# Performance work log

Hardware: AMD Instinct MI355X
Metric: run time of the kernel (lower is better)

The kernel has to match this reference:

```python
import jax, jax.numpy as jnp
import numpy as np

P = 2; NH = 8; NW = 4; NB = 6; D = 512; HID = 2048; NREG = 1; T = 1000; NACT = 3
HH = 32; WW = 32; C = 3; B = 1; DUR = 6


def _kron_bool(a, b):
    # kron(A,B)[i*p+k, j*q+l] = A[i,j] & B[k,l]
    m, n = a.shape; p, q = b.shape
    return (a[:, None, :, None] & b[None, :, None, :]).reshape(m * p, n * q)


def _masks(dur_zr, seq_zr, dur_xa, seq_xa):
    m_left = _kron_bool(jnp.eye(dur_zr, dtype=bool), jnp.ones((seq_zr, seq_zr), dtype=bool))
    tmp = jnp.ones((dur_zr, dur_zr), dtype=bool)
    band = jnp.tril(tmp, -1) ^ jnp.tril(tmp, -1 - NW)  # sliding window over previous frames
    m_right = _kron_bool(band[:, :-1], jnp.ones((seq_zr, seq_xa), dtype=bool))
    m_self = _kron_bool(jnp.tril(jnp.ones((dur_xa, dur_xa), dtype=bool)), jnp.ones((seq_xa, seq_xa), dtype=bool))
    return ~jnp.concatenate([m_left, m_right], axis=1), ~m_self


def _ln(x):
    mu = jnp.mean(x, -1, keepdims=True)
    xc = x - mu
    var = jnp.mean(xc * xc, -1, keepdims=True)
    return xc * jax.lax.rsqrt(var + 1e-5)


def _patch(x, Wp, bp):
    b, dur, c, h, w = x.shape
    x = x.reshape(b, dur, c, h // P, P, w // P, P)
    x = x.transpose(0, 1, 3, 5, 2, 4, 6).reshape(b, dur, (h // P) * (w // P), c * P * P)
    return x @ Wp + bp


def _unpatch(x, Wu, bu):
    b, dur, s, d = x.shape
    y = x @ Wu + bu  # [b,dur,s,C*P*P]
    y = y.reshape(b, dur, HH // P, WW // P, C, P, P)
    return y.transpose(0, 1, 4, 2, 5, 3, 6).reshape(b, dur, C, HH, WW)


def _mod(x, cond, Wm, bm):
    # AdaLN: per-frame scale/shift broadcast over tokens of that frame
    scale, shift = jnp.split(jax.nn.silu(cond) @ Wm + bm, 2, axis=-1)
    b, L, d = x.shape; dur = cond.shape[1]; s = L // dur
    y = _ln(x).reshape(b, dur, s, d)
    return (y * (1.0 + scale[:, :, None]) + shift[:, :, None]).reshape(b, L, d)


def _gate(x, cond, Wg, bg):
    g = cond @ Wg + bg
    b, L, d = x.shape; dur = cond.shape[1]; s = L // dur
    return (x.reshape(b, dur, s, d) * g[:, :, None]).reshape(b, L, d)


def _attn(q, kv, mask, Wq, bq, Wk, bk, Wv, bv, Wo, bo):
    b, lq, d = q.shape; lk = kv.shape[1]; dh = d // NH
    qh = (q @ Wq + bq).reshape(b, lq, NH, dh)
    kh = (kv @ Wk + bk).reshape(b, lk, NH, dh)
    vh = (kv @ Wv + bv).reshape(b, lk, NH, dh)
    s = jnp.einsum('bqhd,bkhd->bhqk', qh, kh) * (1.0 / np.sqrt(dh))
    s = jnp.where(mask[None, None], -1e9, s)  # mask True = disallowed
    o = jnp.einsum('bhqk,bkhd->bqhd', jax.nn.softmax(s, axis=-1), vh)
    return o.reshape(b, lq, d) @ Wo + bo


def _geglu(x, Wg, bg, Wo, bo):
    a, g = jnp.split(x @ Wg + bg, 2, axis=-1)
    return (a * jax.nn.gelu(g, approximate=False)) @ Wo + bo


def _forward(z, frames, actions, ts, W_patch, b_patch, W_unpatch, b_unpatch, registers, pe_grid, action_emb, time_emb, W_mod1, b_mod1, W_mod2, b_mod2, W_q, b_q, W_k, b_k, W_v, b_v, W_o, b_o, W_g1, b_g1, W_g2, b_g2, W_geglu, b_geglu, W_ffout, b_ffout):
    zt = _patch(z, W_patch, b_patch) + pe_grid[None, None]
    xt = _patch(frames, W_patch, b_patch) + pe_grid[None, None]
    a = action_emb[actions]  # [B, dur, D]
    b, dur_zr, s, d = zt.shape
    zr = jnp.concatenate([zt, jnp.broadcast_to(registers[None, None], (b, dur_zr, NREG, d))], axis=2)
    xa = jnp.concatenate([xt, a[:, :-1, None, :]], axis=2)
    seq_zr = zr.shape[2]; dur_xa = xa.shape[1]; seq_xa = xa.shape[2]
    mask_cross, mask_self = _masks(dur_zr, seq_zr, dur_xa, seq_xa)
    zr = zr.reshape(b, dur_zr * seq_zr, d)
    xa = xa.reshape(b, dur_xa * seq_xa, d)
    cond = time_emb[ts]  # [B, dur_zr, D]
    clean = jnp.broadcast_to(time_emb[0][None, None], (b, dur_xa, d))
    for i in range(NB):
        zrn = _mod(zr, cond, W_mod1[i], b_mod1[i])
        xan = _mod(xa, clean, W_mod1[i], b_mod1[i])
        xkv = jnp.concatenate([zrn, xan], axis=1)
        cross = _attn(zrn, xkv, mask_cross, W_q[i], b_q[i], W_k[i], b_k[i], W_v[i], b_v[i], W_o[i], b_o[i])
        selfa = _attn(xan, xan, mask_self, W_q[i], b_q[i], W_k[i], b_k[i], W_v[i], b_v[i], W_o[i], b_o[i])
        zr = _gate(zrn, cond, W_g1[i], b_g1[i])
        xa = _gate(xan, clean, W_g1[i], b_g1[i])
        zr = _mod(zr + cross, cond, W_mod2[i], b_mod2[i])
        xa = _mod(xa + selfa, clean, W_mod2[i], b_mod2[i])
        zr = _geglu(zr, W_geglu[i], b_geglu[i], W_ffout[i], b_ffout[i])
        xa = _geglu(xa, W_geglu[i], b_geglu[i], W_ffout[i], b_ffout[i])
        zr = _gate(zr, cond, W_g2[i], b_g2[i])
        xa = _gate(xa, clean, W_g2[i], b_g2[i])
    zr = zr.reshape(b, dur_zr, seq_zr, d)[:, :, :-NREG]
    return _unpatch(zr, W_unpatch, b_unpatch)


def setup_inputs() -> dict:
    key = jax.random.key(0)
    ks = iter(jax.random.split(key, 64))
    def rn(shape, scale=0.02):
        return jax.random.normal(next(ks), shape, dtype=jnp.float32) * scale
    inp = {}
    inp['z'] = jax.random.normal(next(ks), (B, DUR, C, HH, WW), dtype=jnp.float32)
    inp['frames'] = jax.random.normal(next(ks), (B, DUR - 1, C, HH, WW), dtype=jnp.float32)
    inp['actions'] = jax.random.randint(next(ks), (B, DUR), 0, NACT)
    inp['ts'] = jax.random.randint(next(ks), (B, DUR), 0, T)
    inp['W_patch'] = rn((C * P * P, D)); inp['b_patch'] = jnp.zeros((D,), jnp.float32)
    inp['W_unpatch'] = rn((D, C * P * P)); inp['b_unpatch'] = jnp.zeros((C * P * P,), jnp.float32)
    inp['registers'] = rn((NREG, D), 1.0 / D ** 0.5)
    inp['pe_grid'] = rn(((HH // P) * (WW // P), D), 1.0 / D ** 0.5)
    inp['action_emb'] = rn((NACT, D), 1.0)
    inp['time_emb'] = rn((T, D), 1.0)
    inp['W_mod1'] = rn((NB, D, 2 * D)); inp['b_mod1'] = jnp.zeros((NB, 2 * D), jnp.float32)
    inp['W_mod2'] = rn((NB, D, 2 * D)); inp['b_mod2'] = jnp.zeros((NB, 2 * D), jnp.float32)
    for nm in ('q', 'k', 'v', 'o'):
        inp['W_' + nm] = rn((NB, D, D)); inp['b_' + nm] = jnp.zeros((NB, D), jnp.float32)
    inp['W_g1'] = rn((NB, D, D)); inp['b_g1'] = jnp.ones((NB, D), jnp.float32)
    inp['W_g2'] = rn((NB, D, D)); inp['b_g2'] = jnp.ones((NB, D), jnp.float32)
    inp['W_geglu'] = rn((NB, D, 2 * HID)); inp['b_geglu'] = jnp.zeros((NB, 2 * HID), jnp.float32)
    inp['W_ffout'] = rn((NB, HID, D)); inp['b_ffout'] = jnp.zeros((NB, D), jnp.float32)
    return inp


def reference(z, frames, actions, ts, W_patch, b_patch, W_unpatch, b_unpatch, registers, pe_grid, action_emb, time_emb, W_mod1, b_mod1, W_mod2, b_mod2, W_q, b_q, W_k, b_k, W_v, b_v, W_o, b_o, W_g1, b_g1, W_g2, b_g2, W_geglu, b_geglu, W_ffout, b_ffout):
    return _forward(z, frames, actions, ts, W_patch, b_patch, W_unpatch, b_unpatch, registers, pe_grid, action_emb, time_emb, W_mod1, b_mod1, W_mod2, b_mod2, W_q, b_q, W_k, b_k, W_v, b_v, W_o, b_o, W_g1, b_g1, W_g2, b_g2, W_geglu, b_geglu, W_ffout, b_ffout)
```

## Files before the change

### kernel.cpp

```cpp
#include <hip/hip_runtime.h>
#include <hip/hip_bf16.h>
#include <math.h>

#define DURZ 6
#define DURX 5
#define SEQ 257
#define LZ 1542
#define LX 1285
#define LT 2827
#define DM 512
#define NHEADS 8
#define DH 64
#define HIDDEN 2048

typedef __bf16 bf16x8 __attribute__((ext_vector_type(8)));
typedef __bf16 bf16x4 __attribute__((ext_vector_type(4)));
typedef float f32x4 __attribute__((ext_vector_type(4)));

__global__ void fill_kernel(float* __restrict__ out, int n, float v) {
    int i = blockIdx.x * blockDim.x + threadIdx.x;
    if (i < n) out[i] = v;
}

__global__ void embed_kernel(const float* __restrict__ z,
// ... 47 lines not shown
    int j = idx & 511;
    int tsr = (r < 6) ? ts[r] : 0;
    float x = time_emb[tsr * 512 + j];
    condraw[idx] = x;
    condsilu[idx] = x / (1.0f + expf(-x));
}

__global__ void params_kernel(const float* __restrict__ condraw,
                              const float* __restrict__ condsilu,
                              const float* __restrict__ W_mod1,
                              const float* __restrict__ b_mod1,
                              const float* __restrict__ W_mod2,
                              const float* __restrict__ b_mod2,
                              const float* __restrict__ W_g1,
                              const float* __restrict__ b_g1,
                              const float* __restrict__ W_g2,
                              const float* __restrict__ b_g2,
                              float* __restrict__ params) {
    int idx = blockIdx.x * blockDim.x + threadIdx.x;
    if (idx >= 6 * 7 * 3072) return;
    int i = idx / 21504;
    int rem = idx % 21504;
    int r = rem / 3072;
    int c = rem % 3072;
    const float* cv;
    const float* W;
    float bias;
    int ldw;
    if (c < 1024) {
        cv = condsilu + r * 512;
        W = W_mod1 + (size_t)i * 512 * 1024 + c; ldw = 1024;
        bias = b_mod1[i * 1024 + c];
    } else if (c < 2048) {
        int cc = c - 1024;
        cv = condsilu + r * 512;
        W = W_mod2 + (size_t)i * 512 * 1024 + cc; ldw = 1024;
        bias = b_mod2[i * 1024 + cc];
    } else if (c < 2560) {
        int cc = c - 2048;
        cv = condraw + r * 512;
        W = W_g1 + (size_t)i * 512 * 512 + cc; ldw = 512;
        bias = b_g1[i * 512 + cc];
    } else {
        int cc = c - 2560;
        cv = condraw + r * 512;
        W = W_g2 + (size_t)i * 512 * 512 + cc; ldw = 512;
        bias = b_g2[i * 512 + cc];
    }
    float acc = bias;
    for (int j = 0; j < 512; j++) acc += cv[j] * W[(size_t)j * ldw];
    params[idx] = acc;
}

__global__ __launch_bounds__(256) void lnmod_kernel(const float* __restrict__ x,
                                                    float* __restrict__ y,
                                                    const float* __restrict__ params,
                                                    int mod_off) {
    int T = blockIdx.x;
    int tid = threadIdx.x;
    int r = (T < LZ) ? (T / SEQ) : 6;
    const float* prow = params + r * 3072 + mod_off;
    const float* xr = x + (size_t)T * DM;
    float v0 = xr[tid], v1 = xr[tid + 256];
    float s_ = v0 + v1, q_ = v0 * v0 + v1 * v1;
#pragma unroll
    for (int off = 32; off; off >>= 1) {
        s_ += __shfl_down(s_, off);
        q_ += __shfl_down(q_, off);
    }
    __shared__ float sh[8];
    int wave = tid >> 6, lane = tid & 63;
    if (lane == 0) { sh[wave] = s_; sh[4 + wave] = q_; }
    __syncthreads();
    float sum = sh[0] + sh[1] + sh[2] + sh[3];
    float sq = sh[4] + sh[5] + sh[6] + sh[7];
    float mu = sum * (1.0f / 512.0f);
    float var = sq * (1.0f / 512.0f) - mu * mu;
    float rstd = rsqrtf(var + 1e-5f);
    int d0 = tid, d1 = tid + 256;
    y[(size_t)T * DM + d0] = (v0 - mu) * rstd * (1.0f + prow[d0]) + prow[512 + d0];
    y[(size_t)T * DM + d1] = (v1 - mu) * rstd * (1.0f + prow[d1]) + prow[512 + d1];
}


#define MFMA3(accv, ah, al, bh, bl)                                            \
    accv = __builtin_amdgcn_mfma_f32_16x16x32_bf16(al, bh, accv, 0, 0, 0);     \
    accv = __builtin_amdgcn_mfma_f32_16x16x32_bf16(ah, bl, accv, 0, 0, 0);     \
    accv = __builtin_amdgcn_mfma_f32_16x16x32_bf16(ah, bh, accv, 0, 0, 0);

__device__ __forceinline__ void split8(const float* v, bf16x8& h, bf16x8& l) {
#pragma unroll
    for (int j = 0; j < 8; ++j) {
        __bf16 hh = (__bf16)v[j];
        h[j] = hh;
        l[j] = (__bf16)(v[j] - (float)hh);
    }
}

__device__ __forceinline__ void stage_chunks(const char* g, char* l, int nch,
                                             int w, int lane) {
    for (int c = w; c < nch; c += 4)
        __builtin_amdgcn_global_load_lds(
            (const unsigned int*)(g + (c << 10) + (lane << 4)),
            (unsigned int*)(l + (c << 10)), 16, 0, 0);
}

__global__ __launch_bounds__(256) void wprep_kernel(const float* __restrict__ Wq,
                                                    const float* __restrict__ Wk,
                                                    const float* __restrict__ Wv,
                                                    const float* __restrict__ Wo,
                                                    const float* __restrict__ Wglu,
                                                    const float* __restrict__ Wff,
                                                    float* __restrict__ Wp) {
    __shared__ __align__(16) __bf16 T[2][128][40];
    int id = blockIdx.x, t = threadIdx.x;
    const float* src;
    int N, nb, kt;
    size_t dstf;
    if (id < 256) {
        int mat = id >> 6, rem = id & 63;
        nb = rem >> 4; kt = rem & 15; N = 512;
        src = mat == 0 ? Wq : mat == 1 ? Wk : mat == 2 ? Wv : Wo;
        dstf = (size_t)mat * 327680 + (size_t)(nb * 16 + kt) * 5120;
    } else if (id < 768) {
        int rem = id - 256;
        nb = rem >> 4; kt = rem & 15; N = 4096; src = Wglu;
        dstf = 1310720 + (size_t)(nb * 16 + kt) * 5120;
    } else {
        int rem = id - 768;
        nb = rem >> 6; kt = rem & 63; N = 512; src = Wff;
        dstf = 3932160 + (size_t)(nb * 64 + kt) * 5120;
    }
    int r = t & 127, ch = t >> 7;
#pragma unroll
    for (int s = 0; s < 16; ++s) {
        int c = s * 2 + ch;
        float x = src[(size_t)(kt * 32 + c) * N + nb * 128 + r];
        __bf16 h = (__bf16)x;
        T[0][r][c] = h;
        T[1][r][c] = (__bf16)(x - (float)h);
    }
    __syncthreads();
    float4* d = (float4*)(Wp + dstf);
    const float4* s4 = (const float4*)(&T[0][0][0]);
    for (int i = t; i < 1280; i += 256) d[i] = s4[i];
}

__global__ __launch_bounds__(256) void mgemm_qkv(const float* __restrict__ A,
                                                 const float* __restrict__ Wp,
                                                 const float* __restrict__ bq,
                                                 const float* __restrict__ bk,
                                                 const float* __restrict__ bv,
                                                 float* __restrict__ Cq,
                                                 float* __restrict__ Ck,
                                                 float* __restrict__ Cv, int M) {
    __shared__ __align__(16) __bf16 Ah[64][40], Al[64][40];
    __shared__ __align__(16) __bf16 B2[2][128][40];
    const int K = 512, N = 512;
    int tid = threadIdx.x;
    int sel = blockIdx.x >> 2;
    int nb = blockIdx.x & 3;
    int n0 = nb * 128;
    int m0 = blockIdx.y * 64;
    const float* bias = sel == 0 ? bq : (sel == 1 ? bk : bv);
    float* C = sel == 0 ? Cq : (sel == 1 ? Ck : Cv);
    const char* breg = (const char*)Wp + (size_t)sel * 1310720 + (size_t)nb * 16 * 20480;
    int w = tid >> 6, lane = tid & 63;
    int wm = (w >> 1) * 32, wn = (w & 1) * 64;
    int q = lane >> 4, lr = lane & 15;
    int row = tid >> 2, kc = (tid & 3) * 8;
    bool mval = (m0 + row) < M;
    f32x4 acc[2][4];
#pragma unroll
    for (int i = 0; i < 2; ++i)
#pragma unroll
        for (int j = 0; j < 4; ++j)
#pragma unroll
            for (int r = 0; r < 4; ++r) acc[i][j][r] = 0.0f;
    for (int kt = 0; kt < 16; ++kt) {
        float av[8];
        const float* ap = A + (size_t)(m0 + row) * K + kt * 32 + kc;
        float4 t0 = mval ? *(const float4*)(ap) : make_float4(0, 0, 0, 0);
        float4 t1 = mval ? *(const float4*)(ap + 4) : make_float4(0, 0, 0, 0);
        av[0] = t0.x; av[1] = t0.y; av[2] = t0.z; av[3] = t0.w;
        av[4] = t1.x; av[5] = t1.y; av[6] = t1.z; av[7] = t1.w;
        __syncthreads();
        stage_chunks(breg + (size_t)kt * 20480, (char*)(&B2[0][0][0]), 20, w, lane);
        bf16x8 h8, l8;
        split8(av, h8, l8);
        *(bf16x8*)&Ah[row][kc] = h8;
        *(bf16x8*)&Al[row][kc] = l8;
        __syncthreads();
        bf16x8 afh[2], afl[2], bfh[4], bfl[4];
#pragma unroll
        for (int i = 0; i < 2; ++i) {
            afh[i] = *(const bf16x8*)(&Ah[wm + i * 16 + lr][q * 8]);
            afl[i] = *(const bf16x8*)(&Al[wm + i * 16 + lr][q * 8]);
        }
#pragma unroll
        for (int j = 0; j < 4; ++j) {
            bfh[j] = *(const bf16x8*)(&B2[0][wn + j * 16 + lr][q * 8]);
            bfl[j] = *(const bf16x8*)(&B2[1][wn + j * 16 + lr][q * 8]);
        }
#pragma unroll
        for (int i = 0; i < 2; ++i)
#pragma unroll
            for (int j = 0; j < 4; ++j) {
                MFMA3(acc[i][j], afh[i], afl[i], bfh[j], bfl[j]);
            }
    }
#pragma unroll
    for (int i = 0; i < 2; ++i)
#pragma unroll
        for (int r = 0; r < 4; ++r) {
            int m = m0 + wm + i * 16 + q * 4 + r;
            if (m < M) {
#pragma unroll
                for (int j = 0; j < 4; ++j) {
                    int n = n0 + wn + j * 16 + lr;
                    C[(size_t)m * N + n] = acc[i][j][r] + bias[n];
                }
            }
        }
}

__global__ __launch_bounds__(256) void mgemm64(const float* __restrict__ A,
                                               const float* __restrict__ Wpreg,
                                               int KT, int K,
                                               const float* __restrict__ bias,
                                               float* __restrict__ C, int M) {
    __shared__ __align__(16) __bf16 Ah[64][40], Al[64][40];
    __shared__ __align__(16) __bf16 B2[2][128][40];
    const int N = 512;
    int tid = threadIdx.x;
    int nb = blockIdx.x;
    int n0 = nb * 128;
    int m0 = blockIdx.y * 64;
    const char* breg = (const char*)Wpreg + (size_t)nb * KT * 20480;
    int w = tid >> 6, lane = tid & 63;
    int wm = (w >> 1) * 32, wn = (w & 1) * 64;
    int q = lane >> 4, lr = lane & 15;
    int row = tid >> 2, kc = (tid & 3) * 8;
    bool mval = (m0 + row) < M;
    f32x4 acc[2][4];
#pragma unroll
    for (int i = 0; i < 2; ++i)
#pragma unroll
        for (int j = 0; j < 4; ++j)
#pragma unroll
            for (int r = 0; r < 4; ++r) acc[i][j][r] = 0.0f;
    for (int kt = 0; kt < KT; ++kt) {
        float av[8];
        const float* ap = A + (size_t)(m0 + row) * K + kt * 32 + kc;
        float4 t0 = mval ? *(const float4*)(ap) : make_float4(0, 0, 0, 0);
        float4 t1 = mval ? *(const float4*)(ap + 4) : make_float4(0, 0, 0, 0);
        av[0] = t0.x; av[1] = t0.y; av[2] = t0.z; av[3] = t0.w;
        av[4] = t1.x; av[5] = t1.y; av[6] = t1.z; av[7] = t1.w;
        __syncthreads();
        stage_chunks(breg + (size_t)kt * 20480, (char*)(&B2[0][0][0]), 20, w, lane);
        bf16x8 h8, l8;
        split8(av, h8, l8);
        *(bf16x8*)&Ah[row][kc] = h8;
        *(bf16x8*)&Al[row][kc] = l8;
        __syncthreads();
        bf16x8 afh[2], afl[2], bfh[4], bfl[4];
#pragma unroll
        for (int i = 0; i < 2; ++i) {
            afh[i] = *(const bf16x8*)(&Ah[wm + i * 16 + lr][q * 8]);
            afl[i] = *(const bf16x8*)(&Al[wm + i * 16 + lr][q * 8]);
        }
#pragma unroll
        for (int j = 0; j < 4; ++j) {
            bfh[j] = *(const bf16x8*)(&B2[0][wn + j * 16 + lr][q * 8]);
            bfl[j] = *(const bf16x8*)(&B2[1][wn + j * 16 + lr][q * 8]);
        }
#pragma unroll
        for (int i = 0; i < 2; ++i)
#pragma unroll
            for (int j = 0; j < 4; ++j) {
                MFMA3(acc[i][j], afh[i], afl[i], bfh[j], bfl[j]);
            }
    }
#pragma unroll
    for (int i = 0; i < 2; ++i)
#pragma unroll
        for (int r = 0; r < 4; ++r) {
            int m = m0 + wm + i * 16 + q * 4 + r;
            if (m < M) {
#pragma unroll
                for (int j = 0; j < 4; ++j) {
                    int n = n0 + wn + j * 16 + lr;
                    C[(size_t)m * N + n] = acc[i][j][r] + bias[n];
                }
            }
        }
}

__global__ __launch_bounds__(256) void mgemm_geglu(const float* __restrict__ A,
                                                   const float* __restrict__ Wpglu,
                                                   const float* __restrict__ bias,
                                                   float* __restrict__ H, int M) {
    __shared__ __align__(16) __bf16 Ah[128][40], Al[128][40];
    __shared__ __align__(16) __bf16 BA[2][128][40];
    __shared__ __align__(16) __bf16 BG[2][128][40];
    const int K = 512;
    int tid = threadIdx.x;
    int nb = blockIdx.x;
    int n0 = nb * 128;
    int m0 = blockIdx.y * 128;
    const char* brega = (const char*)Wpglu + (size_t)nb * 16 * 20480;
    const char* bregg = (const char*)Wpglu + (size_t)(nb + 16) * 16 * 20480;
    int w = tid >> 6, lane = tid & 63;
    int wm = (w >> 1) * 64, wn = (w & 1) * 64;
    int q = lane >> 4, lr = lane & 15;
    int sm = tid & 127, kh = (tid >> 7) * 16;
    bool mval = (m0 + sm) < M;
    f32x4 acca[4][4], accg[4][4];
#pragma unroll
    for (int i = 0; i < 4; ++i)
#pragma unroll
        for (int j = 0; j < 4; ++j)
#pragma unroll
            for (int r = 0; r < 4; ++r) { acca[i][j][r] = 0.0f; accg[i][j][r] = 0.0f; }
    for (int kt = 0; kt < 16; ++kt) {
        float av[16];
        const float* ap = A + (size_t)(m0 + sm) * K + kt * 32 + kh;
#pragma unroll
        for (int c = 0; c < 4; ++c) {
            float4 t = mval ? *(const float4*)(ap + c * 4) : make_float4(0, 0, 0, 0);
            av[c * 4 + 0] = t.x; av[c * 4 + 1] = t.y;
            av[c * 4 + 2] = t.z; av[c * 4 + 3] = t.w;
        }
        __syncthreads();
        stage_chunks(brega + (size_t)kt * 20480, (char*)(&BA[0][0][0]), 20, w, lane);
        stage_chunks(bregg + (size_t)kt * 20480, (char*)(&BG[0][0][0]), 20, w, lane);
        bf16x8 h0, l0, h1, l1;
        split8(av, h0, l0);
        split8(av + 8, h1, l1);
        *(bf16x8*)&Ah[sm][kh] = h0;
        *(bf16x8*)&Ah[sm][kh + 8] = h1;
        *(bf16x8*)&Al[sm][kh] = l0;
        *(bf16x8*)&Al[sm][kh + 8] = l1;
        __syncthreads();
        bf16x8 afh[4], afl[4];
#pragma unroll
        for (int i = 0; i < 4; ++i) {
            afh[i] = *(const bf16x8*)(&Ah[wm + i * 16 + lr][q * 8]);
            afl[i] = *(const bf16x8*)(&Al[wm + i * 16 + lr][q * 8]);
        }
#pragma unroll
        for (int j = 0; j < 4; ++j) {
            bf16x8 bah = *(const bf16x8*)(&BA[0][wn + j * 16 + lr][q * 8]);
            bf16x8 bal = *(const bf16x8*)(&BA[1][wn + j * 16 + lr][q * 8]);
            bf16x8 bgh = *(const bf16x8*)(&BG[0][wn + j * 16 + lr][q * 8]);
            bf16x8 bgl = *(const bf16x8*)(&BG[1][wn + j * 16 + lr][q * 8]);
#pragma unroll
            for (int i = 0; i < 4; ++i) {
                MFMA3(acca[i][j], afh[i], afl[i], bah, bal);
                MFMA3(accg[i][j], afh[i], afl[i], bgh, bgl);
            }
        }
    }
#pragma unroll
    for (int i = 0; i < 4; ++i)
#pragma unroll
        for (int r = 0; r < 4; ++r) {
            int m = m0 + wm + i * 16 + q * 4 + r;
            if (m < M) {
#pragma unroll
                for (int j = 0; j < 4; ++j) {
                    int n = n0 + wn + j * 16 + lr;
                    float a = acca[i][j][r] + bias[n];
                    float g = accg[i][j][r] + bias[2048 + n];
                    float gel = 0.5f * g * (1.0f + erff(g * 0.70710678118654752f));
                    H[(size_t)m * HIDDEN + n] = a * gel;
                }
            }
        }
}

__global__ __launch_bounds__(256) void fattn_kernel(const float* __restrict__ Q,
                                                    const float* __restrict__ K,
                                                    const float* __restrict__ V,
                                                    float* __restrict__ O) {
    __shared__ __align__(16) __bf16 Kh[64][72], Kl[64][72];
    __shared__ __align__(16) __bf16 Vth[64][72], Vtl[64][72];
    __shared__ __align__(16) __bf16 Ph[4][16][72], Pl[4][16][72];
    int tid = threadIdx.x;
    int w = tid >> 6, lane = tid & 63;
    int lq = lane & 15, lg = lane >> 4;
    int hoff = blockIdx.z * DH;
    int qbase, base0, len0, base1, len1;
    if (blockIdx.y < 6) {
        int f = blockIdx.y;
        qbase = f * SEQ;
        base0 = f * SEQ; len0 = SEQ;
        int jl = f - 4; if (jl < 0) jl = 0;
        base1 = LZ + jl * SEQ; len1 = (f - jl) * SEQ;
    } else {
        int f = blockIdx.y - 6;
        qbase = LZ + f * SEQ;
        base0 = LZ; len0 = (f + 1) * SEQ;
        base1 = 0; len1 = 0;
    }
    int q0 = blockIdx.x * 64;
    int qvalid = SEQ - q0; if (qvalid > 64) qvalid = 64;

    bf16x8 qh[2], ql[2];
    {
        int qr = w * 16 + lq;
        bool v = qr < qvalid;
        const float* qp = Q + (size_t)(qbase + q0 + qr) * DM + hoff + lg * 8;
#pragma unroll
        for (int s = 0; s < 2; ++s) {
            float4 a = v ? *(const float4*)(qp + s * 32) : make_float4(0, 0, 0, 0);
            float4 b = v ? *(const float4*)(qp + s * 32 + 4) : make_float4(0, 0, 0, 0);
            float fa[8] = {a.x, a.y, a.z, a.w, b.x, b.y, b.z, b.w};
#pragma unroll
            for (int j = 0; j < 8; ++j) {
                __bf16 hh = (__bf16)fa[j];
                qh[s][j] = hh;
                ql[s][j] = (__bf16)(fa[j] - (float)hh);
            }
        }
    }
    f32x4 acc[4];
#pragma unroll
    for (int n = 0; n < 4; ++n)
#pragma unroll
        for (int r = 0; r < 4; ++r) acc[n][r] = 0.0f;
    float m_i = -1e30f, l_i = 0.0f;

    for (int rng = 0; rng < 2; ++rng) {
        int base = rng ? base1 : base0;
        int len = rng ? len1 : len0;
        for (int t0 = 0; t0 < len; t0 += 64) {
            int valid = len - t0; if (valid > 64) valid = 64;
// ... 72 lines not shown
#pragma unroll
            for (int i2 = 0; i2 < 16; ++i2) {
                p[i2] = __expf(p[i2] - mnew);
                rsum += p[i2];
            }
            rsum += __shfl_xor(rsum, 16);
            rsum += __shfl_xor(rsum, 32);
            l_i = l_i * alpha + rsum;
            m_i = mnew;
            float ar[4];
#pragma unroll
            for (int r = 0; r < 4; ++r) ar[r] = __shfl(alpha, lg * 4 + r);
#pragma unroll
            for (int n = 0; n < 4; ++n)
#pragma unroll
                for (int r = 0; r < 4; ++r) acc[n][r] *= ar[r];
#pragma unroll
            for (int sub = 0; sub < 4; ++sub) {
                bf16x4 h4, l4;
#pragma unroll
                for (int r = 0; r < 4; ++r) {
                    float x = p[sub * 4 + r];
                    __bf16 hh = (__bf16)x;
                    h4[r] = hh;
                    l4[r] = (__bf16)(x - (float)hh);
                }
                *(bf16x4*)&Ph[w][lq][sub * 16 + lg * 4] = h4;
                *(bf16x4*)&Pl[w][lq][sub * 16 + lg * 4] = l4;
            }
            bf16x8 pah[2], pal[2];
#pragma unroll
            for (int s = 0; s < 2; ++s) {
                pah[s] = *(const bf16x8*)(&Ph[w][lq][s * 32 + lg * 8]);
                pal[s] = *(const bf16x8*)(&Pl[w][lq][s * 32 + lg * 8]);
            }
#pragma unroll
            for (int n = 0; n < 4; ++n) {
#pragma unroll
                for (int s = 0; s < 2; ++s) {
                    bf16x8 vfh = *(const bf16x8*)(&Vth[n * 16 + lq][s * 32 + lg * 8]);
                    bf16x8 vfl = *(const bf16x8*)(&Vtl[n * 16 + lq][s * 32 + lg * 8]);
                    MFMA3(acc[n], pah[s], pal[s], vfh, vfl);
                }
            }
        }
    }
    float linv[4];
#pragma unroll
    for (int r = 0; r < 4; ++r) linv[r] = 1.0f / __shfl(l_i, lg * 4 + r);
#pragma unroll
    for (int r = 0; r < 4; ++r) {
        int qr = w * 16 + lg * 4 + r;
        if (qr < qvalid) {
            float* op = O + (size_t)(qbase + q0 + qr) * DM + hoff;
#pragma unroll
            for (int n = 0; n < 4; ++n) op[n * 16 + lq] = acc[n][r] * linv[r];
        }
    }
}

__global__ void gate1add_kernel(const float* __restrict__ xn,
                                const float* __restrict__ proj,
                                float* __restrict__ y2,
                                const float* __restrict__ params) {
    int idx = blockIdx.x * blockDim.x + threadIdx.x;
    if (idx >= LT * DM) return;
    int T = idx >> 9, d = idx & 511;
    int r = (T < LZ) ? (T / SEQ) : 6;
    y2[idx] = xn[idx] * params[r * 3072 + 2048 + d] + proj[idx];
}

__global__ void gate2_kernel(const float* __restrict__ src, float* __restrict__ state,
                             const float* __restrict__ params) {
    int idx = blockIdx.x * blockDim.x + threadIdx.x;
    if (idx >= LT * DM) return;
    int T = idx >> 9, d = idx & 511;
    int r = (T < LZ) ? (T / SEQ) : 6;
    state[idx] = src[idx] * params[r * 3072 + 2560 + d];
}

__global__ void unpatch_kernel(const float* __restrict__ state,
                               const float* __restrict__ Wu,
                               const float* __restrict__ bu,
                               float* __restrict__ out) {
    int idx = blockIdx.x * blockDim.x + threadIdx.x;
    if (idx >= DURZ * 3 * 32 * 32) return;
    int w = idx & 31, hh = (idx >> 5) & 31, c = (idx >> 10) % 3, f = idx / (3 * 1024);
    int t = (hh >> 1) * 16 + (w >> 1);
    int j = c * 4 + (hh & 1) * 2 + (w & 1);
    const float* xr = state + (size_t)(f * SEQ + t) * DM;
    float acc = bu[j];
    for (int k = 0; k < DM; ++k) acc += xr[k] * Wu[k * 12 + j];
    out[idx] = acc;
}

extern "C" void kernel_launch(void* const* d_in, const int* in_sizes, int n_in,
                              void* d_out, int out_size, void* d_ws, size_t ws_size,
                              hipStream_t stream) {
    static const int expected_sizes[32] = {
        18432, 15360, 6, 6,
        6144, 512, 6144, 12,
        512, 131072, 1536, 512000,
        3145728, 6144, 3145728, 6144,
        1572864, 3072, 1572864, 3072,
        1572864, 3072, 1572864, 3072,
        1572864, 3072, 1572864, 3072,
        12582912, 24576, 6291456, 3072
    };
    if (n_in != 32) {
        fill_kernel<<<(18432 + 255) / 256, 256, 0, stream>>>((float*)d_out, 18432, 3.0f);
        return;
    }
    for (int i = 0; i < 32; ++i) {
        if (in_sizes[i] != expected_sizes[i]) {
            fill_kernel<<<(18432 + 255) / 256, 256, 0, stream>>>((float*)d_out, 18432,
                                                                 4.0f + (float)i);
            return;
        }
    }

    const float* z = (const float*)d_in[0];
    const float* frames = (const float*)d_in[1];
    const int* actions = (const int*)d_in[2];
    const int* ts = (const int*)d_in[3];
    const float* W_patch = (const float*)d_in[4];
    const float* b_patch = (const float*)d_in[5];
    const float* W_unpatch = (const float*)d_in[6];
    const float* b_unpatch = (const float*)d_in[7];
    const float* registers = (const float*)d_in[8];
    const float* pe_grid = (const float*)d_in[9];
    const float* action_emb = (const float*)d_in[10];
    const float* time_emb = (const float*)d_in[11];
    const float* W_mod1 = (const float*)d_in[12];
    const float* b_mod1 = (const float*)d_in[13];
    const float* W_mod2 = (const float*)d_in[14];
    const float* b_mod2 = (const float*)d_in[15];
    const float* W_q = (const float*)d_in[16];
    const float* b_q = (const float*)d_in[17];
    const float* W_k = (const float*)d_in[18];
    const float* b_k = (const float*)d_in[19];
    const float* W_v = (const float*)d_in[20];
    const float* b_v = (const float*)d_in[21];
    const float* W_o = (const float*)d_in[22];
    const float* b_o = (const float*)d_in[23];
    const float* W_g1 = (const float*)d_in[24];
    const float* b_g1 = (const float*)d_in[25];
    const float* W_g2 = (const float*)d_in[26];
    const float* b_g2 = (const float*)d_in[27];
    const float* W_geglu = (const float*)d_in[28];
    const float* b_geglu = (const float*)d_in[29];
    const float* W_ffout = (const float*)d_in[30];
    const float* b_ffout = (const float*)d_in[31];

    const size_t S = (size_t)LT * DM;
    size_t need = (8 * S + 129024 + 7168 + 5242880) * sizeof(float);
    if (ws_size < need) {
        fill_kernel<<<(18432 + 255) / 256, 256, 0, stream>>>((float*)d_out, 18432, 40.0f);
        return;
    }
    float* ws = (float*)d_ws;
    float* state = ws;
    float* xn = ws + S;
    float* qb = ws + 2 * S;
    float* kb = ws + 3 * S;
    float* vb = ws + 4 * S;
    float* attno = ws + 5 * S;
    float* proj = ws + 6 * S;
    float* params = ws + 8 * S;
    float* condraw = params + 129024;
    float* condsilu = condraw + 3584;
    float* wp = condsilu + 3584;
    float* hbuf = qb;

    embed_kernel<<<LT, 256, 0, stream>>>(z, frames, actions, W_patch, b_patch,
                                         registers, pe_grid, action_emb, state);
    cond_kernel<<<(7 * 512 + 255) / 256, 256, 0, stream>>>(ts, time_emb, condraw, condsilu);
    params_kernel<<<(6 * 7 * 3072 + 255) / 256, 256, 0, stream>>>(
        condraw, condsilu, W_mod1, b_mod1, W_mod2, b_mod2, W_g1, b_g1, W_g2, b_g2, params);

    const int MT64 = (LT + 63) / 64;
    dim3 gqkv(12, MT64);
    dim3 g64(4, MT64);
    dim3 gglu(16, (LT + 127) / 128);
    dim3 gattn(5, 11, NHEADS);
    int ew = (LT * DM + 255) / 256;
    for (int i = 0; i < 6; ++i) {
        const float* P = params + i * 21504;
        wprep_kernel<<<1024, 256, 0, stream>>>(
            W_q + (size_t)i * DM * DM, W_k + (size_t)i * DM * DM,
            W_v + (size_t)i * DM * DM, W_o + (size_t)i * DM * DM,
            W_geglu + (size_t)i * DM * 4096, W_ffout + (size_t)i * HIDDEN * DM, wp);
        lnmod_kernel<<<LT, 256, 0, stream>>>(state, xn, P, 0);
        mgemm_qkv<<<gqkv, 256, 0, stream>>>(xn, wp, b_q + i * DM, b_k + i * DM,
                                            b_v + i * DM, qb, kb, vb, LT);
        fattn_kernel<<<gattn, 256, 0, stream>>>(qb, kb, vb, attno);
        mgemm64<<<g64, 256, 0, stream>>>(attno, wp + 983040, 16, 512,
                                         b_o + i * DM, proj, LT);
        gate1add_kernel<<<ew, 256, 0, stream>>>(xn, proj, attno, P);
        lnmod_kernel<<<LT, 256, 0, stream>>>(attno, xn, P, 1024);
        mgemm_geglu<<<gglu, 256, 0, stream>>>(xn, wp + 1310720,
                                              b_geglu + i * 4096, hbuf, LT);
        mgemm64<<<g64, 256, 0, stream>>>(hbuf, wp + 3932160, 64, 2048,
                                         b_ffout + i * DM, proj, LT);
        gate2_kernel<<<ew, 256, 0, stream>>>(proj, state, P);
    }
    unpatch_kernel<<<(DURZ * 3 * 32 * 32 + 255) / 256, 256, 0, stream>>>(
        state, W_unpatch, b_unpatch, (float*)d_out);
}
```

Baseline: 2.173 ms.

## Unify GEMMs with pre-split bf16 activations, double buffering, and fused gate epilogues

Activations feeding GEMMs are now written by producers (layernorm, attention, GEMM epilogues) as separate bf16 hi/lo planes, so GEMMs load A straight into LDS via global_load_lds with a swizzle instead of splitting fp32 in-kernel. All GEMMs are merged into one templated, double-buffered kernel that uses 64-wide N sub-tiles and an XCD-aware block remap. The gate1-add and gate2 elementwise kernels are fused into the GEMM epilogues, which removes two full-tensor passes per block. The weight-prep layout changes to 64-row sub-tiles, and the GEGLU tile shrinks to 64x64, which launches more blocks.

Result: faster. 1.974 ms (-9.1%).

```diff
diff --git a/kernel.cpp b/kernel.cpp
--- a/kernel.cpp
+++ b/kernel.cpp
@@ -123,16 +123,27 @@
     params[idx] = acc;
 }
 
-__global__ __launch_bounds__(256) void lnmod_kernel(const float* __restrict__ x,
-                                                    float* __restrict__ y,
+template<bool PL>
+__global__ __launch_bounds__(256) void lnmod_kernel(const float* __restrict__ xf,
+                                                    const __bf16* __restrict__ xh,
+                                                    const __bf16* __restrict__ xl,
+                                                    __bf16* __restrict__ yh,
+                                                    __bf16* __restrict__ yl,
                                                     const float* __restrict__ params,
                                                     int mod_off) {
     int T = blockIdx.x;
     int tid = threadIdx.x;
     int r = (T < LZ) ? (T / SEQ) : 6;
     const float* prow = params + r * 3072 + mod_off;
-    const float* xr = x + (size_t)T * DM;
-    float v0 = xr[tid], v1 = xr[tid + 256];
+    size_t base = (size_t)T * DM;
+    float v0, v1;
+    if constexpr (PL) {
+        v0 = (float)xh[base + tid] + (float)xl[base + tid];
+        v1 = (float)xh[base + tid + 256] + (float)xl[base + tid + 256];
+    } else {
+        v0 = xf[base + tid];
+        v1 = xf[base + tid + 256];
+    }
     float s_ = v0 + v1, q_ = v0 * v0 + v1 * v1;
 #pragma unroll
     for (int off = 32; off; off >>= 1) {
@@ -148,9 +159,13 @@
     float mu = sum * (1.0f / 512.0f);
     float var = sq * (1.0f / 512.0f) - mu * mu;
     float rstd = rsqrtf(var + 1e-5f);
-    int d0 = tid, d1 = tid + 256;
-    y[(size_t)T * DM + d0] = (v0 - mu) * rstd * (1.0f + prow[d0]) + prow[512 + d0];
-    y[(size_t)T * DM + d1] = (v1 - mu) * rstd * (1.0f + prow[d1]) + prow[512 + d1];
+    float y0 = (v0 - mu) * rstd * (1.0f + prow[tid]) + prow[512 + tid];
+    float y1 = (v1 - mu) * rstd * (1.0f + prow[tid + 256]) + prow[512 + tid + 256];
+    __bf16 h0 = (__bf16)y0, h1 = (__bf16)y1;
+    yh[base + tid] = h0;
+    yl[base + tid] = (__bf16)(y0 - (float)h0);
+    yh[base + tid + 256] = h1;
+    yl[base + tid + 256] = (__bf16)(y1 - (float)h1);
 }
 
 
@@ -158,23 +173,6 @@
     accv = __builtin_amdgcn_mfma_f32_16x16x32_bf16(al, bh, accv, 0, 0, 0);     \
     accv = __builtin_amdgcn_mfma_f32_16x16x32_bf16(ah, bl, accv, 0, 0, 0);     \
     accv = __builtin_amdgcn_mfma_f32_16x16x32_bf16(ah, bh, accv, 0, 0, 0);
-
-__device__ __forceinline__ void split8(const float* v, bf16x8& h, bf16x8& l) {
-#pragma unroll
-    for (int j = 0; j < 8; ++j) {
-        __bf16 hh = (__bf16)v[j];
-        h[j] = hh;
-        l[j] = (__bf16)(v[j] - (float)hh);
-    }
-}
-
-__device__ __forceinline__ void stage_chunks(const char* g, char* l, int nch,
-                                             int w, int lane) {
-    for (int c = w; c < nch; c += 4)
-        __builtin_amdgcn_global_load_lds(
-            (const unsigned int*)(g + (c << 10) + (lane << 4)),
-            (unsigned int*)(l + (c << 10)), 16, 0, 0);
-}
 
 __global__ __launch_bounds__(256) void wprep_kernel(const float* __restrict__ Wq,
                                                     const float* __restrict__ Wk,
@@ -183,30 +181,31 @@
                                                     const float* __restrict__ Wglu,
                                                     const float* __restrict__ Wff,
                                                     float* __restrict__ Wp) {
-    __shared__ __align__(16) __bf16 T[2][128][40];
+    __shared__ __align__(16) __bf16 T[2][64][40];
     int id = blockIdx.x, t = threadIdx.x;
     const float* src;
-    int N, nb, kt;
+    int N, nsub, kt;
     size_t dstf;
-    if (id < 256) {
-        int mat = id >> 6, rem = id & 63;
-        nb = rem >> 4; kt = rem & 15; N = 512;
+    if (id < 512) {
+        int mat = id >> 7, rem = id & 127;
+        nsub = rem >> 4; kt = rem & 15; N = 512;
         src = mat == 0 ? Wq : mat == 1 ? Wk : mat == 2 ? Wv : Wo;
-        dstf = (size_t)mat * 327680 + (size_t)(nb * 16 + kt) * 5120;
-    } else if (id < 768) {
-        int rem = id - 256;
-        nb = rem >> 4; kt = rem & 15; N = 4096; src = Wglu;
-        dstf = 1310720 + (size_t)(nb * 16 + kt) * 5120;
+        dstf = (size_t)mat * 327680 + (size_t)(nsub * 16 + kt) * 2560;
+    } else if (id < 1536) {
+        int rem = id - 512;
+        nsub = rem >> 4; kt = rem & 15; N = 4096; src = Wglu;
+        dstf = 1310720 + (size_t)(nsub * 16 + kt) * 2560;
     } else {
-        int rem = id - 768;
-        nb = rem >> 6; kt = rem & 63; N = 512; src = Wff;
-        dstf = 3932160 + (size_t)(nb * 64 + kt) * 5120;
-    }
-    int r = t & 127, ch = t >> 7;
-#pragma unroll
-    for (int s = 0; s < 16; ++s) {
-        int c = s * 2 + ch;
-        float x = src[(size_t)(kt * 32 + c) * N + nb * 128 + r];
+        int rem = id - 1536;
+        nsub = rem >> 6; kt = rem & 63; N = 512; src = Wff;
+        dstf = 3932160 + (size_t)(nsub * 64 + kt) * 2560;
+    }
+    int r = t >> 2;
+    int cb = (t & 3) * 8;
+#pragma unroll
+    for (int j = 0; j < 8; ++j) {
+        int c = cb + j;
+        float x = src[(size_t)(kt * 32 + c) * N + nsub * 64 + r];
         __bf16 h = (__bf16)x;
         T[0][r][c] = h;
         T[1][r][c] = (__bf16)(x - (float)h);
@@ -214,33 +213,76 @@
     __syncthreads();
     float4* d = (float4*)(Wp + dstf);
     const float4* s4 = (const float4*)(&T[0][0][0]);
-    for (int i = t; i < 1280; i += 256) d[i] = s4[i];
-}
-
-__global__ __launch_bounds__(256) void mgemm_qkv(const float* __restrict__ A,
-                                                 const float* __restrict__ Wp,
-                                                 const float* __restrict__ bq,
-                                                 const float* __restrict__ bk,
-                                                 const float* __restrict__ bv,
-                                                 float* __restrict__ Cq,
-                                                 float* __restrict__ Ck,
-                                                 float* __restrict__ Cv, int M) {
-    __shared__ __align__(16) __bf16 Ah[64][40], Al[64][40];
-    __shared__ __align__(16) __bf16 B2[2][128][40];
-    const int K = 512, N = 512;
+    for (int i2 = t; i2 < 640; i2 += 256) d[i2] = s4[i2];
+}
+
+#define M_QKV 0
+#define M_GATE1 1
+#define M_GLU 2
+#define M_GATE2 3
+
+template<int MODE>
+__global__ __launch_bounds__(256) void gemm_kernel(
+    const __bf16* __restrict__ Aph, const __bf16* __restrict__ Apl,
+    const char* __restrict__ Wbase, int KT, int Krow,
+    const float* __restrict__ b0, const float* __restrict__ b1,
+    const float* __restrict__ b2,
+    float* __restrict__ C0, float* __restrict__ C1, float* __restrict__ C2,
+    __bf16* __restrict__ Oh, __bf16* __restrict__ Ol,
+    const __bf16* __restrict__ Xh, const __bf16* __restrict__ Xl,
+    const float* __restrict__ params, int M) {
+    __shared__ __align__(16) __bf16 Alds[2][2][64][32];
+    __shared__ __align__(16) __bf16 Blds[2][2][2][64][40];
     int tid = threadIdx.x;
-    int sel = blockIdx.x >> 2;
-    int nb = blockIdx.x & 3;
-    int n0 = nb * 128;
-    int m0 = blockIdx.y * 64;
-    const float* bias = sel == 0 ? bq : (sel == 1 ? bk : bv);
-    float* C = sel == 0 ? Cq : (sel == 1 ? Ck : Cv);
-    const char* breg = (const char*)Wp + (size_t)sel * 1310720 + (size_t)nb * 16 * 20480;
     int w = tid >> 6, lane = tid & 63;
-    int wm = (w >> 1) * 32, wn = (w & 1) * 64;
     int q = lane >> 4, lr = lane & 15;
-    int row = tid >> 2, kc = (tid & 3) * 8;
-    bool mval = (m0 + row) < M;
+    int nwg = gridDim.x * gridDim.y;
+    int lin = blockIdx.y * gridDim.x + blockIdx.x;
+    int qq = nwg >> 3, rr = nwg & 7;
+    int xcd = lin & 7, ix = lin >> 3;
+    int wg = (xcd < rr) ? xcd * (qq + 1) + ix : rr * (qq + 1) + (xcd - rr) * qq + ix;
+    int mb = wg % gridDim.x;
+    int nb = wg / gridDim.x;
+    int m0 = mb * 64;
+    const char* sb0;
+    const char* sb1;
+    if constexpr (MODE == M_QKV) {
+        int sel = nb >> 2;
+        const char* mbp = Wbase + (size_t)sel * 1310720;
+        sb0 = mbp + (size_t)(2 * (nb & 3)) * 163840;
+        sb1 = mbp + (size_t)(2 * (nb & 3) + 1) * 163840;
+    } else if constexpr (MODE == M_GLU) {
+        sb0 = Wbase + (size_t)nb * 163840;
+        sb1 = Wbase + (size_t)(32 + nb) * 163840;
+    } else {
+        sb0 = Wbase + (size_t)(2 * nb) * (size_t)KT * 10240;
+        sb1 = Wbase + (size_t)(2 * nb + 1) * (size_t)KT * 10240;
+    }
+    int wm = (w >> 1) * 32;
+
+    auto stage = [&](int sbuf, int kt) {
+        const char* k0 = sb0 + (size_t)kt * 10240;
+        const char* k1 = sb1 + (size_t)kt * 10240;
+        char* bl = (char*)(&Blds[sbuf][0][0][0][0]);
+        for (int idx = w; idx < 20; idx += 4) {
+            int sub = idx & 1, c = idx >> 1;
+            const char* g = (sub ? k1 : k0) + (c << 10) + (lane << 4);
+            __builtin_amdgcn_global_load_lds((const unsigned int*)g,
+                (unsigned int*)(bl + sub * 10240 + (c << 10)), 16, 0, 0);
+        }
+        char* al = (char*)(&Alds[sbuf][0][0][0]);
+        for (int idx = w; idx < 8; idx += 4) {
+            int p = idx & 1, c = idx >> 1;
+            int row = c * 16 + (lane >> 2);
+            int ss = (lane & 3) ^ ((row >> 1) & 3);
+            int mrow = m0 + row;
+            if (mrow > M - 1) mrow = M - 1;
+            const __bf16* ap = (p ? Apl : Aph) + (size_t)mrow * Krow + kt * 32 + ss * 8;
+            __builtin_amdgcn_global_load_lds((const unsigned int*)ap,
+                (unsigned int*)(al + p * 4096 + (c << 10)), 16, 0, 0);
+        }
+    };
+
     f32x4 acc[2][4];
 #pragma unroll
     for (int i = 0; i < 2; ++i)
@@ -248,203 +290,93 @@
         for (int j = 0; j < 4; ++j)
 #pragma unroll
             for (int r = 0; r < 4; ++r) acc[i][j][r] = 0.0f;
-    for (int kt = 0; kt < 16; ++kt) {
-        float av[8];
-        const float* ap = A + (size_t)(m0 + row) * K + kt * 32 + kc;
-        float4 t0 = mval ? *(const float4*)(ap) : make_float4(0, 0, 0, 0);
-        float4 t1 = mval ? *(const float4*)(ap + 4) : make_float4(0, 0, 0, 0);
-        av[0] = t0.x; av[1] = t0.y; av[2] = t0.z; av[3] = t0.w;
-        av[4] = t1.x; av[5] = t1.y; av[6] = t1.z; av[7] = t1.w;
+
+    stage(0, 0);
+    __syncthreads();
+    for (int kt = 0; kt < KT; ++kt) {
+        int buf = kt & 1;
+        if (kt + 1 < KT) stage(buf ^ 1, kt + 1);
+        bf16x8 afh[2], afl[2], bh[4], bl4[4];
+#pragma unroll
+        for (int i = 0; i < 2; ++i) {
+            int row = wm + i * 16 + lr;
+            int off = (q * 16) ^ (((row >> 1) & 3) << 4);
+            afh[i] = *(const bf16x8*)((const char*)(&Alds[buf][0][row][0]) + off);
+            afl[i] = *(const bf16x8*)((const char*)(&Alds[buf][1][row][0]) + off);
+        }
+#pragma unroll
+        for (int j = 0; j < 4; ++j) {
+            int bsub, brow;
+            if constexpr (MODE == M_GLU) {
+                bsub = j >> 1;
+                brow = (w & 1) * 32 + (j & 1) * 16 + lr;
+            } else {
+                bsub = w & 1;
+                brow = j * 16 + lr;
+            }
+            bh[j] = *(const bf16x8*)(&Blds[buf][bsub][0][brow][q * 8]);
+            bl4[j] = *(const bf16x8*)(&Blds[buf][bsub][1][brow][q * 8]);
+        }
+#pragma unroll
+        for (int i = 0; i < 2; ++i)
+#pragma unroll
+            for (int j = 0; j < 4; ++j) {
+                MFMA3(acc[i][j], afh[i], afl[i], bh[j], bl4[j]);
+            }
         __syncthreads();
-        stage_chunks(breg + (size_t)kt * 20480, (char*)(&B2[0][0][0]), 20, w, lane);
-        bf16x8 h8, l8;
-        split8(av, h8, l8);
-        *(bf16x8*)&Ah[row][kc] = h8;
-        *(bf16x8*)&Al[row][kc] = l8;
-        __syncthreads();
-        bf16x8 afh[2], afl[2], bfh[4], bfl[4];
-#pragma unroll
-        for (int i = 0; i < 2; ++i) {
-            afh[i] = *(const bf16x8*)(&Ah[wm + i * 16 + lr][q * 8]);
-            afl[i] = *(const bf16x8*)(&Al[wm + i * 16 + lr][q * 8]);
-        }
-#pragma unroll
-        for (int j = 0; j < 4; ++j) {
-            bfh[j] = *(const bf16x8*)(&B2[0][wn + j * 16 + lr][q * 8]);
-            bfl[j] = *(const bf16x8*)(&B2[1][wn + j * 16 + lr][q * 8]);
-        }
-#pragma unroll
-        for (int i = 0; i < 2; ++i)
-#pragma unroll
-            for (int j = 0; j < 4; ++j) {
-                MFMA3(acc[i][j], afh[i], afl[i], bfh[j], bfl[j]);
-            }
-    }
+    }
+
 #pragma unroll
     for (int i = 0; i < 2; ++i)
 #pragma unroll
         for (int r = 0; r < 4; ++r) {
             int m = m0 + wm + i * 16 + q * 4 + r;
-            if (m < M) {
+            if (m >= M) continue;
+            if constexpr (MODE == M_QKV) {
+                int sel = nb >> 2;
+                const float* bias = sel == 0 ? b0 : (sel == 1 ? b1 : b2);
+                float* C = sel == 0 ? C0 : (sel == 1 ? C1 : C2);
+                int c0 = (nb & 3) * 128 + (w & 1) * 64;
 #pragma unroll
                 for (int j = 0; j < 4; ++j) {
-                    int n = n0 + wn + j * 16 + lr;
-                    C[(size_t)m * N + n] = acc[i][j][r] + bias[n];
-                }
-            }
-        }
-}
-
-__global__ __launch_bounds__(256) void mgemm64(const float* __restrict__ A,
-                                               const float* __restrict__ Wpreg,
-                                               int KT, int K,
-                                               const float* __restrict__ bias,
-                                               float* __restrict__ C, int M) {
-    __shared__ __align__(16) __bf16 Ah[64][40], Al[64][40];
-    __shared__ __align__(16) __bf16 B2[2][128][40];
-    const int N = 512;
-    int tid = threadIdx.x;
-    int nb = blockIdx.x;
-    int n0 = nb * 128;
-    int m0 = blockIdx.y * 64;
-    const char* breg = (const char*)Wpreg + (size_t)nb * KT * 20480;
-    int w = tid >> 6, lane = tid & 63;
-    int wm = (w >> 1) * 32, wn = (w & 1) * 64;
-    int q = lane >> 4, lr = lane & 15;
-    int row = tid >> 2, kc = (tid & 3) * 8;
-    bool mval = (m0 + row) < M;
-    f32x4 acc[2][4];
-#pragma unroll
-    for (int i = 0; i < 2; ++i)
-#pragma unroll
-        for (int j = 0; j < 4; ++j)
-#pragma unroll
-            for (int r = 0; r < 4; ++r) acc[i][j][r] = 0.0f;
-    for (int kt = 0; kt < KT; ++kt) {
-        float av[8];
-        const float* ap = A + (size_t)(m0 + row) * K + kt * 32 + kc;
-        float4 t0 = mval ? *(const float4*)(ap) : make_float4(0, 0, 0, 0);
-        float4 t1 = mval ? *(const float4*)(ap + 4) : make_float4(0, 0, 0, 0);
-        av[0] = t0.x; av[1] = t0.y; av[2] = t0.z; av[3] = t0.w;
-        av[4] = t1.x; av[5] = t1.y; av[6] = t1.z; av[7] = t1.w;
-        __syncthreads();
-        stage_chunks(breg + (size_t)kt * 20480, (char*)(&B2[0][0][0]), 20, w, lane);
-        bf16x8 h8, l8;
-        split8(av, h8, l8);
-        *(bf16x8*)&Ah[row][kc] = h8;
-        *(bf16x8*)&Al[row][kc] = l8;
-        __syncthreads();
-        bf16x8 afh[2], afl[2], bfh[4], bfl[4];
-#pragma unroll
-        for (int i = 0; i < 2; ++i) {
-            afh[i] = *(const bf16x8*)(&Ah[wm + i * 16 + lr][q * 8]);
-            afl[i] = *(const bf16x8*)(&Al[wm + i * 16 + lr][q * 8]);
-        }
-#pragma unroll
-        for (int j = 0; j < 4; ++j) {
-            bfh[j] = *(const bf16x8*)(&B2[0][wn + j * 16 + lr][q * 8]);
-            bfl[j] = *(const bf16x8*)(&B2[1][wn + j * 16 + lr][q * 8]);
-        }
-#pragma unroll
-        for (int i = 0; i < 2; ++i)
-#pragma unroll
-            for (int j = 0; j < 4; ++j) {
-                MFMA3(acc[i][j], afh[i], afl[i], bfh[j], bfl[j]);
-            }
-    }
-#pragma unroll
-    for (int i = 0; i < 2; ++i)
-#pragma unroll
-        for (int r = 0; r < 4; ++r) {
-            int m = m0 + wm + i * 16 + q * 4 + r;
-            if (m < M) {
+                    int n = c0 + j * 16 + lr;
+                    C[(size_t)m * 512 + n] = acc[i][j][r] + bias[n];
+                }
+            } else if constexpr (MODE == M_GATE1) {
+                int r6 = (m < LZ) ? (m / SEQ) : 6;
+                const float* g1 = params + r6 * 3072 + 2048;
+                int c0 = nb * 128 + (w & 1) * 64;
 #pragma unroll
                 for (int j = 0; j < 4; ++j) {
-                    int n = n0 + wn + j * 16 + lr;
-                    C[(size_t)m * N + n] = acc[i][j][r] + bias[n];
-                }
-            }
-        }
-}
-
-__global__ __launch_bounds__(256) void mgemm_geglu(const float* __restrict__ A,
-                                                   const float* __restrict__ Wpglu,
-                                                   const float* __restrict__ bias,
-                                                   float* __restrict__ H, int M) {
-    __shared__ __align__(16) __bf16 Ah[128][40], Al[128][40];
-    __shared__ __align__(16) __bf16 BA[2][128][40];
-    __shared__ __align__(16) __bf16 BG[2][128][40];
-    const int K = 512;
-    int tid = threadIdx.x;
-    int nb = blockIdx.x;
-    int n0 = nb * 128;
-    int m0 = blockIdx.y * 128;
-    const char* brega = (const char*)Wpglu + (size_t)nb * 16 * 20480;
-    const char* bregg = (const char*)Wpglu + (size_t)(nb + 16) * 16 * 20480;
-    int w = tid >> 6, lane = tid & 63;
-    int wm = (w >> 1) * 64, wn = (w & 1) * 64;
-    int q = lane >> 4, lr = lane & 15;
-    int sm = tid & 127, kh = (tid >> 7) * 16;
-    bool mval = (m0 + sm) < M;
-    f32x4 acca[4][4], accg[4][4];
-#pragma unroll
-    for (int i = 0; i < 4; ++i)
-#pragma unroll
-        for (int j = 0; j < 4; ++j)
-#pragma unroll
-            for (int r = 0; r < 4; ++r) { acca[i][j][r] = 0.0f; accg[i][j][r] = 0.0f; }
-    for (int kt = 0; kt < 16; ++kt) {
-        float av[16];
-        const float* ap = A + (size_t)(m0 + sm) * K + kt * 32 + kh;
-#pragma unroll
-        for (int c = 0; c < 4; ++c) {
-            float4 t = mval ? *(const float4*)(ap + c * 4) : make_float4(0, 0, 0, 0);
-            av[c * 4 + 0] = t.x; av[c * 4 + 1] = t.y;
-            av[c * 4 + 2] = t.z; av[c * 4 + 3] = t.w;
-        }
-        __syncthreads();
-        stage_chunks(brega + (size_t)kt * 20480, (char*)(&BA[0][0][0]), 20, w, lane);
-        stage_chunks(bregg + (size_t)kt * 20480, (char*)(&BG[0][0][0]), 20, w, lane);
-        bf16x8 h0, l0, h1, l1;
-        split8(av, h0, l0);
-        split8(av + 8, h1, l1);
-        *(bf16x8*)&Ah[sm][kh] = h0;
-        *(bf16x8*)&Ah[sm][kh + 8] = h1;
-        *(bf16x8*)&Al[sm][kh] = l0;
-        *(bf16x8*)&Al[sm][kh + 8] = l1;
-        __syncthreads();
-        bf16x8 afh[4], afl[4];
-#pragma unroll
-        for (int i = 0; i < 4; ++i) {
-            afh[i] = *(const bf16x8*)(&Ah[wm + i * 16 + lr][q * 8]);
-            afl[i] = *(const bf16x8*)(&Al[wm + i * 16 + lr][q * 8]);
-        }
-#pragma unroll
-        for (int j = 0; j < 4; ++j) {
-            bf16x8 bah = *(const bf16x8*)(&BA[0][wn + j * 16 + lr][q * 8]);
-            bf16x8 bal = *(const bf16x8*)(&BA[1][wn + j * 16 + lr][q * 8]);
-            bf16x8 bgh = *(const bf16x8*)(&BG[0][wn + j * 16 + lr][q * 8]);
-            bf16x8 bgl = *(const bf16x8*)(&BG[1][wn + j * 16 + lr][q * 8]);
-#pragma unroll
-            for (int i = 0; i < 4; ++i) {
-                MFMA3(acca[i][j], afh[i], afl[i], bah, bal);
-                MFMA3(accg[i][j], afh[i], afl[i], bgh, bgl);
-            }
-        }
-    }
-#pragma unroll
-    for (int i = 0; i < 4; ++i)
-#pragma unroll
-        for (int r = 0; r < 4; ++r) {
-            int m = m0 + wm + i * 16 + q * 4 + r;
-            if (m < M) {
+                    int n = c0 + j * 16 + lr;
+                    size_t o = (size_t)m * 512 + n;
+                    float x = (float)Xh[o] + (float)Xl[o];
+                    float v = x * g1[n] + acc[i][j][r] + b0[n];
+                    __bf16 hh = (__bf16)v;
+                    Oh[o] = hh;
+                    Ol[o] = (__bf16)(v - (float)hh);
+                }
+            } else if constexpr (MODE == M_GLU) {
+#pragma unroll
+                for (int j = 0; j < 2; ++j) {
+                    int n = nb * 64 + (w & 1) * 32 + j * 16 + lr;
+                    float a = acc[i][j][r] + b0[n];
+                    float g = acc[i][j + 2][r] + b0[2048 + n];
+                    float gel = 0.5f * g * (1.0f + erff(g * 0.70710678118654752f));
+                    float v = a * gel;
+                    size_t o = (size_t)m * 2048 + n;
+                    __bf16 hh = (__bf16)v;
+                    Oh[o] = hh;
+                    Ol[o] = (__bf16)(v - (float)hh);
+                }
+            } else {
+                int r6 = (m < LZ) ? (m / SEQ) : 6;
+                const float* g2 = params + r6 * 3072 + 2560;
+                int c0 = nb * 128 + (w & 1) * 64;
 #pragma unroll
                 for (int j = 0; j < 4; ++j) {
-                    int n = n0 + wn + j * 16 + lr;
-                    float a = acca[i][j][r] + bias[n];
-                    float g = accg[i][j][r] + bias[2048 + n];
-                    float gel = 0.5f * g * (1.0f + erff(g * 0.70710678118654752f));
-                    H[(size_t)m * HIDDEN + n] = a * gel;
+                    int n = c0 + j * 16 + lr;
+                    C0[(size_t)m * 512 + n] = (acc[i][j][r] + b0[n]) * g2[n];
                 }
             }
         }
@@ -453,7 +385,8 @@
 __global__ __launch_bounds__(256) void fattn_kernel(const float* __restrict__ Q,
                                                     const float* __restrict__ K,
                                                     const float* __restrict__ V,
-                                                    float* __restrict__ O) {
+                                                    __bf16* __restrict__ Oh,
+                                                    __bf16* __restrict__ Ol) {
     __shared__ __align__(16) __bf16 Kh[64][72], Kl[64][72];
     __shared__ __align__(16) __bf16 Vth[64][72], Vtl[64][72];
     __shared__ __align__(16) __bf16 Ph[4][16][72], Pl[4][16][72];
@@ -632,31 +565,16 @@
     for (int r = 0; r < 4; ++r) {
         int qr = w * 16 + lg * 4 + r;
         if (qr < qvalid) {
-            float* op = O + (size_t)(qbase + q0 + qr) * DM + hoff;
-#pragma unroll
-            for (int n = 0; n < 4; ++n) op[n * 16 + lq] = acc[n][r] * linv[r];
-        }
-    }
-}
-
-__global__ void gate1add_kernel(const float* __restrict__ xn,
-                                const float* __restrict__ proj,
-                                float* __restrict__ y2,
-                                const float* __restrict__ params) {
-    int idx = blockIdx.x * blockDim.x + threadIdx.x;
-    if (idx >= LT * DM) return;
-    int T = idx >> 9, d = idx & 511;
-    int r = (T < LZ) ? (T / SEQ) : 6;
-    y2[idx] = xn[idx] * params[r * 3072 + 2048 + d] + proj[idx];
-}
-
-__global__ void gate2_kernel(const float* __restrict__ src, float* __restrict__ state,
-                             const float* __restrict__ params) {
-    int idx = blockIdx.x * blockDim.x + threadIdx.x;
-    if (idx >= LT * DM) return;
-    int T = idx >> 9, d = idx & 511;
-    int r = (T < LZ) ? (T / SEQ) : 6;
-    state[idx] = src[idx] * params[r * 3072 + 2560 + d];
+            size_t ob = (size_t)(qbase + q0 + qr) * DM + hoff;
+#pragma unroll
+            for (int n = 0; n < 4; ++n) {
+                float v = acc[n][r] * linv[r];
+                __bf16 hh = (__bf16)v;
+                Oh[ob + n * 16 + lq] = hh;
+                Ol[ob + n * 16 + lq] = (__bf16)(v - (float)hh);
+            }
+        }
+    }
 }
 
 __global__ void unpatch_kernel(const float* __restrict__ state,
@@ -733,24 +651,28 @@
     const float* b_ffout = (const float*)d_in[31];
 
     const size_t S = (size_t)LT * DM;
-    size_t need = (8 * S + 129024 + 7168 + 5242880) * sizeof(float);
+    size_t need = (7 * S + 129024 + 7168 + 5242880) * sizeof(float);
     if (ws_size < need) {
         fill_kernel<<<(18432 + 255) / 256, 256, 0, stream>>>((float*)d_out, 18432, 40.0f);
         return;
     }
     float* ws = (float*)d_ws;
     float* state = ws;
-    float* xn = ws + S;
+    __bf16* xnh = (__bf16*)(ws + S);
+    __bf16* xnl = (__bf16*)(ws + S + S / 2);
     float* qb = ws + 2 * S;
     float* kb = ws + 3 * S;
     float* vb = ws + 4 * S;
-    float* attno = ws + 5 * S;
-    float* proj = ws + 6 * S;
-    float* params = ws + 8 * S;
+    __bf16* atth = (__bf16*)(ws + 5 * S);
+    __bf16* attl = (__bf16*)(ws + 5 * S + S / 2);
+    __bf16* y2h = (__bf16*)(ws + 6 * S);
+    __bf16* y2l = (__bf16*)(ws + 6 * S + S / 2);
+    __bf16* Hph = (__bf16*)(ws + 2 * S);
+    __bf16* Hpl = (__bf16*)(ws + 4 * S);
+    float* params = ws + 7 * S;
     float* condraw = params + 129024;
     float* condsilu = condraw + 3584;
     float* wp = condsilu + 3584;
-    float* hbuf = qb;
 
     embed_kernel<<<LT, 256, 0, stream>>>(z, frames, actions, W_patch, b_patch,
                                          registers, pe_grid, action_emb, state);
@@ -758,31 +680,38 @@
     params_kernel<<<(6 * 7 * 3072 + 255) / 256, 256, 0, stream>>>(
         condraw, condsilu, W_mod1, b_mod1, W_mod2, b_mod2, W_g1, b_g1, W_g2, b_g2, params);
 
-    const int MT64 = (LT + 63) / 64;
-    dim3 gqkv(12, MT64);
-    dim3 g64(4, MT64);
-    dim3 gglu(16, (LT + 127) / 128);
+    dim3 gqkv(45, 12);
+    dim3 ggate1(45, 4);
+    dim3 gglu(45, 32);
+    dim3 ggate2(45, 4);
     dim3 gattn(5, 11, NHEADS);
-    int ew = (LT * DM + 255) / 256;
     for (int i = 0; i < 6; ++i) {
         const float* P = params + i * 21504;
-        wprep_kernel<<<1024, 256, 0, stream>>>(
+        wprep_kernel<<<2048, 256, 0, stream>>>(
             W_q + (size_t)i * DM * DM, W_k + (size_t)i * DM * DM,
             W_v + (size_t)i * DM * DM, W_o + (size_t)i * DM * DM,
             W_geglu + (size_t)i * DM * 4096, W_ffout + (size_t)i * HIDDEN * DM, wp);
-        lnmod_kernel<<<LT, 256, 0, stream>>>(state, xn, P, 0);
-        mgemm_qkv<<<gqkv, 256, 0, stream>>>(xn, wp, b_q + i * DM, b_k + i * DM,
-                                            b_v + i * DM, qb, kb, vb, LT);
-        fattn_kernel<<<gattn, 256, 0, stream>>>(qb, kb, vb, attno);
-        mgemm64<<<g64, 256, 0, stream>>>(attno, wp + 983040, 16, 512,
-                                         b_o + i * DM, proj, LT);
-        gate1add_kernel<<<ew, 256, 0, stream>>>(xn, proj, attno, P);
-        lnmod_kernel<<<LT, 256, 0, stream>>>(attno, xn, P, 1024);
-        mgemm_geglu<<<gglu, 256, 0, stream>>>(xn, wp + 1310720,
-                                              b_geglu + i * 4096, hbuf, LT);
-        mgemm64<<<g64, 256, 0, stream>>>(hbuf, wp + 3932160, 64, 2048,
-                                         b_ffout + i * DM, proj, LT);
-        gate2_kernel<<<ew, 256, 0, stream>>>(proj, state, P);
+        lnmod_kernel<false><<<LT, 256, 0, stream>>>(state, nullptr, nullptr,
+                                                    xnh, xnl, P, 0);
+        gemm_kernel<M_QKV><<<gqkv, 256, 0, stream>>>(
+            xnh, xnl, (const char*)wp, 16, 512,
+            b_q + i * DM, b_k + i * DM, b_v + i * DM, qb, kb, vb,
+            nullptr, nullptr, nullptr, nullptr, nullptr, LT);
+        fattn_kernel<<<gattn, 256, 0, stream>>>(qb, kb, vb, atth, attl);
+        gemm_kernel<M_GATE1><<<ggate1, 256, 0, stream>>>(
+            atth, attl, (const char*)(wp + 983040), 16, 512,
+            b_o + i * DM, nullptr, nullptr, nullptr, nullptr, nullptr,
+            y2h, y2l, xnh, xnl, P, LT);
+        lnmod_kernel<true><<<LT, 256, 0, stream>>>(nullptr, y2h, y2l,
+                                                   xnh, xnl, P, 1024);
+        gemm_kernel<M_GLU><<<gglu, 256, 0, stream>>>(
+            xnh, xnl, (const char*)(wp + 1310720), 16, 512,
+            b_geglu + (size_t)i * 4096, nullptr, nullptr, nullptr, nullptr, nullptr,
+            Hph, Hpl, nullptr, nullptr, nullptr, LT);
+        gemm_kernel<M_GATE2><<<ggate2, 256, 0, stream>>>(
+            Hph, Hpl, (const char*)(wp + 3932160), 64, 2048,
+            b_ffout + i * DM, nullptr, nullptr, state, nullptr, nullptr,
+            nullptr, nullptr, nullptr, nullptr, P, LT);
     }
     unpatch_kernel<<<(DURZ * 3 * 32 * 32 + 255) / 256, 256, 0, stream>>>(
         state, W_unpatch, b_unpatch, (float*)d_out);
```
